# Optimization experiments

Hardware: AMD Instinct MI355X
Metric: run time of the kernel (lower is better)

The kernel has to match this reference:

```python
import jax, jax.numpy as jnp
import numpy as np

S = 4096       # sequence length
D = 1024       # d_model
H = 16         # heads
DK = 64        # d_k == d_v
VERY_SMOL_NUM = -1e9


def setup_inputs() -> dict:
    key = jax.random.key(0)
    ks = jax.random.split(key, 14)
    sd = 1.0 / np.sqrt(D)
    inp = {
        "V": jax.random.normal(ks[0], (S, D), jnp.float32),
        "K": jax.random.normal(ks[1], (S, D), jnp.float32),
        "Q": jax.random.normal(ks[2], (S, D), jnp.float32),
        # per-head projection weights, stored [in, out] (x @ W + b)
        "WQ": jax.random.normal(ks[3], (H, D, DK), jnp.float32) * sd,
        "bQ": jax.random.normal(ks[4], (H, DK), jnp.float32) * sd,
        "WK": jax.random.normal(ks[5], (H, D, DK), jnp.float32) * sd,
        "bK": jax.random.normal(ks[6], (H, DK), jnp.float32) * sd,
        "WV": jax.random.normal(ks[7], (H, D, DK), jnp.float32) * sd,
        "bV": jax.random.normal(ks[8], (H, DK), jnp.float32) * sd,
        "WO": jax.random.normal(ks[9], (D, D), jnp.float32) * sd,
        "bO": jax.random.normal(ks[10], (D,), jnp.float32) * sd,
    }
    return inp


def reference(V, K, Q, WQ, bQ, WK, bK, WV, bV, WO, bO):
    # per-head projections, vectorized over heads: [H, S, DK]
    q = jnp.einsum('sd,hdk->hsk', Q, WQ) + bQ[:, None, :]
    k = jnp.einsum('sd,hdk->hsk', K, WK) + bK[:, None, :]
    v = jnp.einsum('sd,hdk->hsk', V, WV) + bV[:, None, :]
    # full QK^T per head, scaled
    scores = jnp.einsum('hsk,htk->hst', q, k) / jnp.sqrt(jnp.float32(DK))
    # original bug faithfully preserved: with masked=True the causal additive
    # mask (triu(ones,1) * VERY_SMOL_NUM) is applied TWICE
    tri = jnp.triu(jnp.ones((S, S), jnp.float32), 1) * VERY_SMOL_NUM
    scores = scores + 2.0 * tri
    # torch Softmax(dim=1) on 2D [S,S] scores == softmax over keys (last dim)
    attn = jax.nn.softmax(scores, axis=-1)
    heads = jnp.einsum('hst,htv->hsv', attn, v)          # [H, S, DK]
    cat = heads.transpose(1, 0, 2).reshape(S, H * DK)    # concat over heads
    return cat @ WO + bO
```

## Files before the change

### kernel.cpp

```cpp
#include <hip/hip_runtime.h>

typedef unsigned short u16;
typedef unsigned int u32;
typedef __attribute__((ext_vector_type(8))) __bf16 bf16x8;
typedef __attribute__((ext_vector_type(4))) float f32x4;
typedef __attribute__((ext_vector_type(16))) float f32x16;

#define S_LEN 4096
#define D_MODEL 1024
#define NH 16
#define DHEAD 64

__device__ __forceinline__ u16 f2bf(float f){
  unsigned u = __float_as_uint(f);
  u += 0x7FFFu + ((u >> 16) & 1u);
  return (u16)(u >> 16);
}

__device__ __forceinline__ void gload_lds16(const void* g, void* l){
  __builtin_amdgcn_global_load_lds((const __attribute__((address_space(1))) void*)g,
                                   (__attribute__((address_space(3))) void*)l, 16, 0, 0);
}

__global__ __launch_bounds__(256) void cvt3_kernel(const float* __restrict__ q,
                                                   const float* __restrict__ k,
                                                   const float* __restrict__ v,
                                                   u16* __restrict__ oq,
                                                   u16* __restrict__ ok,
                                                   u16* __restrict__ ov){
  int z = blockIdx.y;
  const float* in = (z==0)? q : (z==1)? k : v;
  u16* out = (z==0)? oq : (z==1)? ok : ov;
  int i = blockIdx.x*256 + threadIdx.x;
  float4 w = reinterpret_cast<const float4*>(in)[i];
  ushort4 o;
  o.x = f2bf(w.x); o.y = f2bf(w.y); o.z = f2bf(w.z); o.w = f2bf(w.w);
  reinterpret_cast<ushort4*>(out)[i] = o;
}

__global__ __launch_bounds__(256) void tcvt_qkv_kernel(const float* __restrict__ wq,
                                                       const float* __restrict__ wk,
                                                       const float* __restrict__ wv,
                                                       u16* __restrict__ oq,
                                                       u16* __restrict__ ok,
                                                       u16* __restrict__ ov){
  int which = blockIdx.y;
  const float* in = (which==0)? wq : (which==1)? wk : wv;
  u16* out = (which==0)? oq : (which==1)? ok : ov;
  __shared__ float tile[64][67];
  int z = blockIdx.z;
  const float* inh = in + (size_t)z*1024*64;
  u16* outh = out + (size_t)z*1024*64;
  int tid = threadIdx.x;
  int r0 = blockIdx.x*64;
  #pragma unroll
  for (int c=0;c<4;c++){
    int cl = c*256 + tid;
    int row = cl >> 4, cc = (cl & 15) * 4;
    float4 v = *reinterpret_cast<const float4*>(inh + (size_t)(r0+row)*64 + cc);
    tile[row][cc+0]=v.x; tile[row][cc+1]=v.y; tile[row][cc+2]=v.z; tile[row][cc+3]=v.w;
  }
  __syncthreads();
  #pragma unroll
  for (int c=0;c<4;c++){
    int cl = c*256 + tid;
    int crow = cl >> 4, rc = (cl & 15) * 4;
    ushort4 o;
    o.x = f2bf(tile[rc+0][crow]);
    o.y = f2bf(tile[rc+1][crow]);
    o.z = f2bf(tile[rc+2][crow]);
    o.w = f2bf(tile[rc+3][crow]);
    *reinterpret_cast<ushort4*>(outh + (size_t)crow*1024 + r0 + rc) = o;
  }
}

__global__ __launch_bounds__(256) void tcvt_wo_kernel(const float* __restrict__ in,
                                                      u16* __restrict__ out){
  __shared__ float tile[64][67];
  int r0 = blockIdx.x*64, c0 = blockIdx.y*64;
  int tid = threadIdx.x;
  #pragma unroll
  for (int c=0;c<4;c++){
    int cl = c*256 + tid;
    int row = cl >> 4, cc = (cl & 15) * 4;
    float4 v = *reinterpret_cast<const float4*>(in + (size_t)(r0+row)*1024 + c0 + cc);
    tile[row][cc+0]=v.x; tile[row][cc+1]=v.y; tile[row][cc+2]=v.z; tile[row][cc+3]=v.w;
  }
  __syncthreads();
  #pragma unroll
  for (int c=0;c<4;c++){
    int cl = c*256 + tid;
    int crow = cl >> 4, rc = (cl & 15) * 4;
    ushort4 o;
    o.x = f2bf(tile[rc+0][crow]);
    o.y = f2bf(tile[rc+1][crow]);
    o.z = f2bf(tile[rc+2][crow]);
    o.w = f2bf(tile[rc+3][crow]);
    *reinterpret_cast<ushort4*>(out + (size_t)(c0+crow)*1024 + r0 + rc) = o;
  }
}

__global__ __launch_bounds__(512) void gemm_qkv_kernel(
    const u16* __restrict__ Qb, const u16* __restrict__ Kb, const u16* __restrict__ Vb,
    const u16* __restrict__ WtQ, const u16* __restrict__ WtK, const u16* __restrict__ WtV,
    const float* __restrict__ bQ, const float* __restrict__ bK, const float* __restrict__ bV,
    u16* __restrict__ qbuf, u16* __restrict__ kbuf, u16* __restrict__ vtb, float qscale){
  const int M = S_LEN, N = D_MODEL, K = D_MODEL;
  int z = blockIdx.z;
  const u16* A  = (z==0)? Qb  : (z==1)? Kb  : Vb;
  const u16* Bt = (z==0)? WtQ : (z==1)? WtK : WtV;
  const float* bias = (z==0)? bQ : (z==1)? bK : bV;
  float oscale = (z==0)? qscale : 1.0f;

  __shared__ __align__(16) unsigned char lsA[2][16384];
  __shared__ __align__(16) unsigned char lsB[2][16384];
  int tid = threadIdx.x;
  int bm = blockIdx.y * 128, bn = blockIdx.x * 128;
  int wave = tid >> 6, lane = tid & 63;
  int wm = (wave >> 1) * 32, wn = (wave & 1) * 64;
  int lrow = lane & 15, lgrp = lane >> 4;

  f32x4 acc[2][4] = {};

  auto STAGE = [&](int buf, int k0){
    #pragma unroll
    for (int c=0;c<4;c++){
      int id = c*512 + tid;
      int r = (id & 1023) >> 3;
      int kc = id & 7;
      int cs = (kc ^ (r & 7)) << 3;
      if (id < 1024)
        gload_lds16(A + (size_t)(bm+r)*K + k0 + cs, lsA[buf] + ((id & 1023) << 4));
      else
        gload_lds16(Bt + (size_t)(bn+r)*K + k0 + cs, lsB[buf] + ((id & 1023) << 4));
    }
  };

  STAGE(0, 0);
  int cur = 0;
  for (int k0 = 0; k0 < K; k0 += 64){
    __syncthreads();
    if (k0 + 64 < K) STAGE(cur^1, k0 + 64);
    #pragma unroll
    for (int ks=0;ks<2;ks++){
      bf16x8 af[2], bfr[4];
      #pragma unroll
      for (int i=0;i<2;i++){
        int ar = wm + i*16 + lrow;
        af[i] = *reinterpret_cast<const bf16x8*>(lsA[cur] + ((ar*128 + ks*64 + lgrp*16) ^ ((ar&7)<<4)));
      }
      #pragma unroll
      for (int j=0;j<4;j++){
        int br = wn + j*16 + lrow;
        bfr[j] = *reinterpret_cast<const bf16x8*>(lsB[cur] + ((br*128 + ks*64 + lgrp*16) ^ ((br&7)<<4)));
      }
      __builtin_amdgcn_s_setprio(1);
      #pragma unroll
      for (int i=0;i<2;i++)
        #pragma unroll
        for (int j=0;j<4;j++)
          acc[i][j] = __builtin_amdgcn_mfma_f32_16x16x32_bf16(af[i], bfr[j], acc[i][j], 0,0,0);
      __builtin_amdgcn_s_setprio(0);
    }
    cur ^= 1;
  }

  #pragma unroll
  for (int j=0;j<4;j++){
    int n = bn + wn + j*16 + lrow;
    float bv = bias[n];
    int hh = n >> 6, kk = n & 63;
    #pragma unroll
    for (int i=0;i<2;i++){
      int m0 = bm + wm + i*16 + lgrp*4;
      float v[4];
      #pragma unroll
      for (int r=0;r<4;r++) v[r] = (acc[i][j][r] + bv) * oscale;
      if (z < 2){
        u16* o = (z==0)? qbuf : kbuf;
        #pragma unroll
        for (int r=0;r<4;r++) o[((size_t)hh*M + m0 + r)*64 + kk] = f2bf(v[r]);
      } else {
        ushort4 p; p.x=f2bf(v[0]); p.y=f2bf(v[1]); p.z=f2bf(v[2]); p.w=f2bf(v[3]);
        *reinterpret_cast<ushort4*>(vtb + ((size_t)hh*64 + kk)*M + m0) = p;
      }
    }
  }
}

__global__ __launch_bounds__(512) void gemm_out_kernel(const u16* __restrict__ A,
                                                       const u16* __restrict__ Bt,
                                                       const float* __restrict__ bias,
                                                       float* __restrict__ dst,
                                                       int M, int N, int K){
  __shared__ __align__(16) unsigned char lsA[2][16384];
  __shared__ __align__(16) unsigned char lsB[2][16384];
  int tid = threadIdx.x;
  int bm = blockIdx.y * 128, bn = blockIdx.x * 128;
  int wave = tid >> 6, lane = tid & 63;
  int wm = (wave >> 1) * 32, wn = (wave & 1) * 64;
  int lrow = lane & 15, lgrp = lane >> 4;

  f32x4 acc[2][4] = {};

  auto STAGE = [&](int buf, int k0){
    #pragma unroll
    for (int c=0;c<4;c++){
      int id = c*512 + tid;
      int r = (id & 1023) >> 3;
      int kc = id & 7;
      int cs = (kc ^ (r & 7)) << 3;
      if (id < 1024)
        gload_lds16(A + (size_t)(bm+r)*K + k0 + cs, lsA[buf] + ((id & 1023) << 4));
      else
        gload_lds16(Bt + (size_t)(bn+r)*K + k0 + cs, lsB[buf] + ((id & 1023) << 4));
    }
  };

  STAGE(0, 0);
  int cur = 0;
  for (int k0 = 0; k0 < K; k0 += 64){
    __syncthreads();
    if (k0 + 64 < K) STAGE(cur^1, k0 + 64);
    #pragma unroll
    for (int ks=0;ks<2;ks++){
      bf16x8 af[2], bfr[4];
      #pragma unroll
      for (int i=0;i<2;i++){
        int ar = wm + i*16 + lrow;
        af[i] = *reinterpret_cast<const bf16x8*>(lsA[cur] + ((ar*128 + ks*64 + lgrp*16) ^ ((ar&7)<<4)));
      }
      #pragma unroll
      for (int j=0;j<4;j++){
        int br = wn + j*16 + lrow;
        bfr[j] = *reinterpret_cast<const bf16x8*>(lsB[cur] + ((br*128 + ks*64 + lgrp*16) ^ ((br&7)<<4)));
      }
      __builtin_amdgcn_s_setprio(1);
      #pragma unroll
      for (int i=0;i<2;i++)
        #pragma unroll
        for (int j=0;j<4;j++)
          acc[i][j] = __builtin_amdgcn_mfma_f32_16x16x32_bf16(af[i], bfr[j], acc[i][j], 0,0,0);
      __builtin_amdgcn_s_setprio(0);
    }
    cur ^= 1;
  }

  #pragma unroll
  for (int j=0;j<4;j++){
    int n = bn + wn + j*16 + lrow;
    float bv = bias[n];
    #pragma unroll
    for (int i=0;i<2;i++){
      int m0 = bm + wm + i*16 + lgrp*4;
      #pragma unroll
      for (int r=0;r<4;r++) dst[(size_t)(m0+r)*N + n] = acc[i][j][r] + bv;
    }
  }
}

__global__ __launch_bounds__(512, 2) void flash_attn_kernel(const u16* __restrict__ qb,
                                                            const u16* __restrict__ kb,
                                                            const u16* __restrict__ vtb,
                                                            u16* __restrict__ pO,
                                                            float2* __restrict__ pml){
  int b = blockIdx.x;
  int h = b & 15;
  int u = b >> 4;
  int qt = 15 - (u >> 2);
  int quarter = u & 3;
  int seg = qt + 1;
  int j0 = quarter * seg, j1 = j0 + seg;

  int tid = threadIdx.x, wave = tid >> 6, lane = tid & 63;
  int l31 = lane & 31, hi = lane >> 5;
  const u16* qh  = qb  + (size_t)h * S_LEN * 64;
  const u16* kh  = kb  + (size_t)h * S_LEN * 64;
  const u16* vth = vtb + (size_t)h * 64 * S_LEN;

  __shared__ __align__(16) unsigned char lsK[2][8192];
  __shared__ __align__(16) unsigned char lsV[2][8192];

  int qw = qt*256 + wave*32;

  bf16x8 qf[4];
  #pragma unroll
  for (int ks=0;ks<4;ks++)
    qf[ks] = *reinterpret_cast<const bf16x8*>(qh + (size_t)(qw + l31)*64 + ks*16 + hi*8);

  f32x16 oacc0 = {}, oacc1 = {};
  float m_run = -3e38f, l_run = 0.f;

  const int kvbase = hi*1024 + l31*16;
  const int krow = tid & 63, kcol = (tid >> 6) << 3;

  auto STAGE = [&](int buf, int jj){
    int kv0 = jj*64;
    gload_lds16(kh + (size_t)(kv0 + krow)*64 + kcol, lsK[buf] + (tid << 4));
    gload_lds16(vth + (size_t)krow*S_LEN + kv0 + kcol, lsV[buf] + (tid << 4));
  };

  STAGE(0, j0);
  int cur = 0;
  for (int j = j0; j < j1; j++){
    __syncthreads();
    if (j + 1 < j1) STAGE(cur^1, j + 1);

    int kv0 = j*64;
    int rel0 = qw - kv0;
    int rel1 = rel0 - 32;
    if (rel0 >= 0){
      bool act1 = rel1 >= 0;
      const unsigned char* Kc = lsK[cur] + kvbase;
      const unsigned char* Vc = lsV[cur] + kvbase;

      f32x16 s0 = {}, s1 = {};
      __builtin_amdgcn_s_setprio(1);
      #pragma unroll
      for (int ks=0;ks<4;ks++){
        bf16x8 kf = *reinterpret_cast<const bf16x8*>(Kc + ks*2048);
        s0 = __builtin_amdgcn_mfma_f32_32x32x16_bf16(kf, qf[ks], s0, 0,0,0);
      }
      if (act1){
        #pragma unroll
        for (int ks=0;ks<4;ks++){
          bf16x8 kf = *reinterpret_cast<const bf16x8*>(Kc + ks*2048 + 512);
          s1 = __builtin_amdgcn_mfma_f32_32x32x16_bf16(kf, qf[ks], s1, 0,0,0);
        }
      }
      __builtin_amdgcn_s_setprio(0);

      if (rel0 == 0){
        #pragma unroll
        for (int reg=0;reg<16;reg++){
          int kvloc = (reg & 3) + 8*(reg >> 2) + 4*hi;
          if (kvloc > l31) s0[reg] = -3e38f;
        }
      }
      if (act1 && rel1 == 0){
        #pragma unroll
        for (int reg=0;reg<16;reg++){
          int kvloc = (reg & 3) + 8*(reg >> 2) + 4*hi;
          if (kvloc > l31) s1[reg] = -3e38f;
        }
      }

      float tm[8];
      #pragma unroll
      for (int i=0;i<8;i++) tm[i] = fmaxf(s0[i], s0[i+8]);
      if (act1){
        #pragma unroll
        for (int i=0;i<8;i++) tm[i] = fmaxf(tm[i], fmaxf(s1[i], s1[i+8]));
      }
      #pragma unroll
      for (int st=4; st>=1; st>>=1){
        #pragma unroll
        for (int i=0;i<st;i++) tm[i] = fmaxf(tm[i], tm[i+st]);
      }
      float mx = fmaxf(tm[0], __shfl_xor(tm[0], 32));

      if (!__all(mx <= m_run + 11.54f)){
        float mnew = fmaxf(m_run, mx);
        float al = __builtin_amdgcn_exp2f(m_run - mnew);
        m_run = mnew; l_run *= al;
        #pragma unroll
        for (int reg=0;reg<16;reg++){ oacc0[reg] *= al; oacc1[reg] *= al; }
      }

      #pragma unroll
      for (int reg=0;reg<16;reg++) s0[reg] = __builtin_amdgcn_exp2f(s0[reg] - m_run);
      if (act1){
        #pragma unroll
        for (int reg=0;reg<16;reg++) s1[reg] = __builtin_amdgcn_exp2f(s1[reg] - m_run);
      }
      float tp[8];
      #pragma unroll
      for (int i=0;i<8;i++) tp[i] = s0[i] + s0[i+8];
      if (act1){
        #pragma unroll
        for (int i=0;i<8;i++) tp[i] += s1[i] + s1[i+8];
      }
      #pragma unroll
      for (int st=4; st>=1; st>>=1){
        #pragma unroll
        for (int i=0;i<st;i++) tp[i] += tp[i+st];
      }
      l_run += tp[0] + __shfl_xor(tp[0], 32);

      #pragma unroll
      for (int b01=0;b01<2;b01++){
        u32 A,B,C,D;
        asm("v_cvt_pk_bf16_f32 %0, %1, %2" : "=v"(A) : "v"(s0[8*b01+0]), "v"(s0[8*b01+1]));
        asm("v_cvt_pk_bf16_f32 %0, %1, %2" : "=v"(B) : "v"(s0[8*b01+2]), "v"(s0[8*b01+3]));
        asm("v_cvt_pk_bf16_f32 %0, %1, %2" : "=v"(C) : "v"(s0[8*b01+4]), "v"(s0[8*b01+5]));
        asm("v_cvt_pk_bf16_f32 %0, %1, %2" : "=v"(D) : "v"(s0[8*b01+6]), "v"(s0[8*b01+7]));
        asm("v_permlane32_swap_b32 %0, %1" : "+v"(A), "+v"(C));
        asm("v_permlane32_swap_b32 %0, %1" : "+v"(B), "+v"(D));
        union { u32 w[4]; bf16x8 v; } U;
        U.w[0]=A; U.w[1]=B; U.w[2]=C; U.w[3]=D;
        bf16x8 vf0 = *reinterpret_cast<const bf16x8*>(Vc + b01*2048);
        bf16x8 vf1 = *reinterpret_cast<const bf16x8*>(Vc + b01*2048 + 512);
        __builtin_amdgcn_s_setprio(1);
        oacc0 = __builtin_amdgcn_mfma_f32_32x32x16_bf16(vf0, U.v, oacc0, 0,0,0);
        oacc1 = __builtin_amdgcn_mfma_f32_32x32x16_bf16(vf1, U.v, oacc1, 0,0,0);
        __builtin_amdgcn_s_setprio(0);
      }
      if (act1){
        #pragma unroll
        for (int b01=0;b01<2;b01++){
          u32 A,B,C,D;
          asm("v_cvt_pk_bf16_f32 %0, %1, %2" : "=v"(A) : "v"(s1[8*b01+0]), "v"(s1[8*b01+1]));
          asm("v_cvt_pk_bf16_f32 %0, %1, %2" : "=v"(B) : "v"(s1[8*b01+2]), "v"(s1[8*b01+3]));
          asm("v_cvt_pk_bf16_f32 %0, %1, %2" : "=v"(C) : "v"(s1[8*b01+4]), "v"(s1[8*b01+5]));
          asm("v_cvt_pk_bf16_f32 %0, %1, %2" : "=v"(D) : "v"(s1[8*b01+6]), "v"(s1[8*b01+7]));
          asm("v_permlane32_swap_b32 %0, %1" : "+v"(A), "+v"(C));
          asm("v_permlane32_swap_b32 %0, %1" : "+v"(B), "+v"(D));
          union { u32 w[4]; bf16x8 v; } U;
          U.w[0]=A; U.w[1]=B; U.w[2]=C; U.w[3]=D;
          bf16x8 vf0 = *reinterpret_cast<const bf16x8*>(Vc + (2+b01)*2048);
          bf16x8 vf1 = *reinterpret_cast<const bf16x8*>(Vc + (2+b01)*2048 + 512);
          __builtin_amdgcn_s_setprio(1);
          oacc0 = __builtin_amdgcn_mfma_f32_32x32x16_bf16(vf0, U.v, oacc0, 0,0,0);
          oacc1 = __builtin_amdgcn_mfma_f32_32x32x16_bf16(vf1, U.v, oacc1, 0,0,0);
          __builtin_amdgcn_s_setprio(0);
        }
      }
    }
    cur ^= 1;
  }

  int q = qw + l31;
  if (hi == 0){
    float2 ml; ml.x = m_run; ml.y = l_run;
    pml[((size_t)quarter*NH + h)*S_LEN + q] = ml;
  }
  #pragma unroll
  for (int df=0;df<2;df++){
    #pragma unroll
    for (int q4=0;q4<4;q4++){
      float a0 = df ? oacc1[4*q4+0] : oacc0[4*q4+0];
      float a1 = df ? oacc1[4*q4+1] : oacc0[4*q4+1];
      float a2 = df ? oacc1[4*q4+2] : oacc0[4*q4+2];
      float a3 = df ? oacc1[4*q4+3] : oacc0[4*q4+3];
      u32 w0d, w1d;
      asm("v_cvt_pk_bf16_f32 %0, %1, %2" : "=v"(w0d) : "v"(a0), "v"(a1));
      asm("v_cvt_pk_bf16_f32 %0, %1, %2" : "=v"(w1d) : "v"(a2), "v"(a3));
      int dquad = df*8 + 2*q4 + hi;
      uint2 pv; pv.x = w0d; pv.y = w1d;
      *reinterpret_cast<uint2*>(pO + (((size_t)(quarter*NH + h)*16 + dquad)*S_LEN + q)*4) = pv;
    }
  }
}

__global__ __launch_bounds__(256) void combine_kernel(const u16* __restrict__ pO,
                                                      const float2* __restrict__ pml,
                                                      u16* __restrict__ catb){
  int tid = threadIdx.x;
  int dq = tid & 15, qo = tid >> 4;
  int h = blockIdx.y;
  int q = blockIdx.x*16 + qo;
  float2 ml[4];
  #pragma unroll
  for (int i=0;i<4;i++) ml[i] = pml[((size_t)i*NH + h)*S_LEN + q];
  float m = fmaxf(fmaxf(ml[0].x, ml[1].x), fmaxf(ml[2].x, ml[3].x));
  float w[4], denom = 0.f;
  #pragma unroll
  for (int i=0;i<4;i++){ w[i] = __builtin_amdgcn_exp2f(ml[i].x - m); denom += w[i]*ml[i].y; }
  float inv = 1.0f / denom;
  float x0=0.f, x1=0.f, x2=0.f, x3=0.f;
  #pragma unroll
  for (int i=0;i<4;i++){
    ushort4 a = reinterpret_cast<const ushort4*>(pO)[((size_t)i*NH*16 + (size_t)h*16 + dq)*S_LEN + q];
    x0 += __uint_as_float((u32)a.x << 16) * w[i];
    x1 += __uint_as_float((u32)a.y << 16) * w[i];
    x2 += __uint_as_float((u32)a.z << 16) * w[i];
    x3 += __uint_as_float((u32)a.w << 16) * w[i];
  }
  ushort4 o;
  o.x = f2bf(x0*inv); o.y = f2bf(x1*inv); o.z = f2bf(x2*inv); o.w = f2bf(x3*inv);
  *reinterpret_cast<ushort4*>(catb + (size_t)q*D_MODEL + h*64 + dq*4) = o;
}

extern "C" void kernel_launch(void* const* d_in, const int* in_sizes, int n_in,
                              void* d_out, int out_size, void* d_ws, size_t ws_size,
                              hipStream_t stream){
  (void)in_sizes; (void)n_in; (void)out_size; (void)ws_size;
  const float* V  = (const float*)d_in[0];
  const float* Km = (const float*)d_in[1];
  const float* Q  = (const float*)d_in[2];
  const float* WQ = (const float*)d_in[3];
  const float* bQ = (const float*)d_in[4];
  const float* WK = (const float*)d_in[5];
  const float* bK = (const float*)d_in[6];
  const float* WV = (const float*)d_in[7];
  const float* bV = (const float*)d_in[8];
  const float* WO = (const float*)d_in[9];
  const float* bO = (const float*)d_in[10];
  float* out = (float*)d_out;

  char* ws = (char*)d_ws;
  const size_t SZ_SD = (size_t)S_LEN * D_MODEL * 2;
  const size_t SZ_W  = (size_t)D_MODEL * D_MODEL * 2;
  u16* Qb   = (u16*)(ws);
  u16* Kb   = (u16*)(ws + SZ_SD);
  u16* Vb   = (u16*)(ws + 2*SZ_SD);
  u16* WtQ  = (u16*)(ws + 3*SZ_SD);
  u16* WtK  = (u16*)(ws + 3*SZ_SD + SZ_W);
  u16* WtV  = (u16*)(ws + 3*SZ_SD + 2*SZ_W);
  u16* WtO  = (u16*)(ws + 3*SZ_SD + 3*SZ_W);
  u16* qbuf = (u16*)(ws + 3*SZ_SD + 4*SZ_W);
  u16* kbuf = (u16*)(ws + 4*SZ_SD + 4*SZ_W);
  u16* vtb  = (u16*)(ws + 5*SZ_SD + 4*SZ_W);
  u16* catb = (u16*)(ws + 6*SZ_SD + 4*SZ_W);
  u16* pO   = (u16*)(ws + 7*SZ_SD + 4*SZ_W);
  float2* pml = (float2*)(ws + 11*SZ_SD + 4*SZ_W);

  const float QSCALE = 0.18033688011112042f;

  cvt3_kernel<<<dim3(4096,3),256,0,stream>>>(Q, Km, V, Qb, Kb, Vb);
  tcvt_qkv_kernel<<<dim3(16,3,16),256,0,stream>>>(WQ, WK, WV, WtQ, WtK, WtV);
  tcvt_wo_kernel<<<dim3(16,16),256,0,stream>>>(WO, WtO);
  gemm_qkv_kernel<<<dim3(8,32,3),512,0,stream>>>(Qb, Kb, Vb, WtQ, WtK, WtV,
                                                 bQ, bK, bV, qbuf, kbuf, vtb, QSCALE);
  flash_attn_kernel<<<dim3(1024),512,0,stream>>>(qbuf, kbuf, vtb, pO, pml);
  combine_kernel<<<dim3(256,16),256,0,stream>>>(pO, pml, catb);
  gemm_out_kernel<<<dim3(8,32),512,0,stream>>>(catb, WtO, bO, out, S_LEN, D_MODEL, D_MODEL);
}
```

Baseline: 153.6 us.

## Fuse fp32-to-bf16 input conversion into QKV GEMM and merge weight transposes

Drops the separate cvt3 pass over Q/K/V. The QKV GEMM now loads fp32 A tiles into registers, converts them with packed bf16 instructions and writes them to LDS, while B still streams via direct global-to-LDS loads. The three weight transpose kernels are merged into one launch. This saves a full read and write of the bf16 activation copies and two kernel launches. In exchange the GEMM reads A in fp32, which is twice the bytes, once per N-block, and uses more registers for the staged values.

```diff
diff --git a/kernel.cpp b/kernel.cpp
--- a/kernel.cpp
+++ b/kernel.cpp
@@ -22,68 +22,31 @@
                                    (__attribute__((address_space(3))) void*)l, 16, 0, 0);
 }
 
-__global__ __launch_bounds__(256) void cvt3_kernel(const float* __restrict__ q,
-                                                   const float* __restrict__ k,
-                                                   const float* __restrict__ v,
-                                                   u16* __restrict__ oq,
-                                                   u16* __restrict__ ok,
-                                                   u16* __restrict__ ov){
-  int z = blockIdx.y;
-  const float* in = (z==0)? q : (z==1)? k : v;
-  u16* out = (z==0)? oq : (z==1)? ok : ov;
-  int i = blockIdx.x*256 + threadIdx.x;
-  float4 w = reinterpret_cast<const float4*>(in)[i];
-  ushort4 o;
-  o.x = f2bf(w.x); o.y = f2bf(w.y); o.z = f2bf(w.z); o.w = f2bf(w.w);
-  reinterpret_cast<ushort4*>(out)[i] = o;
-}
-
-__global__ __launch_bounds__(256) void tcvt_qkv_kernel(const float* __restrict__ wq,
+__global__ __launch_bounds__(256) void tcvt_all_kernel(const float* __restrict__ wq,
                                                        const float* __restrict__ wk,
                                                        const float* __restrict__ wv,
+                                                       const float* __restrict__ wo,
                                                        u16* __restrict__ oq,
                                                        u16* __restrict__ ok,
-                                                       u16* __restrict__ ov){
-  int which = blockIdx.y;
-  const float* in = (which==0)? wq : (which==1)? wk : wv;
-  u16* out = (which==0)? oq : (which==1)? ok : ov;
+                                                       u16* __restrict__ ov,
+                                                       u16* __restrict__ oo){
   __shared__ float tile[64][67];
-  int z = blockIdx.z;
-  const float* inh = in + (size_t)z*1024*64;
-  u16* outh = out + (size_t)z*1024*64;
+  int y = blockIdx.y, z = blockIdx.z, x = blockIdx.x;
+  int r0 = x*64, c0;
+  const float* in; u16* out; int inStride;
+  if (y < 3){
+    in  = ((y==0)? wq : (y==1)? wk : wv) + (size_t)z*1024*64;
+    out = ((y==0)? oq : (y==1)? ok : ov) + (size_t)z*1024*64;
+    c0 = 0; inStride = 64;
+  } else {
+    in = wo; out = oo; c0 = z*64; inStride = 1024;
+  }
   int tid = threadIdx.x;
-  int r0 = blockIdx.x*64;
   #pragma unroll
   for (int c=0;c<4;c++){
     int cl = c*256 + tid;
     int row = cl >> 4, cc = (cl & 15) * 4;
-    float4 v = *reinterpret_cast<const float4*>(inh + (size_t)(r0+row)*64 + cc);
-    tile[row][cc+0]=v.x; tile[row][cc+1]=v.y; tile[row][cc+2]=v.z; tile[row][cc+3]=v.w;
-  }
-  __syncthreads();
-  #pragma unroll
-  for (int c=0;c<4;c++){
-    int cl = c*256 + tid;
-    int crow = cl >> 4, rc = (cl & 15) * 4;
-    ushort4 o;
-    o.x = f2bf(tile[rc+0][crow]);
-    o.y = f2bf(tile[rc+1][crow]);
-    o.z = f2bf(tile[rc+2][crow]);
-    o.w = f2bf(tile[rc+3][crow]);
-    *reinterpret_cast<ushort4*>(outh + (size_t)crow*1024 + r0 + rc) = o;
-  }
-}
-
-__global__ __launch_bounds__(256) void tcvt_wo_kernel(const float* __restrict__ in,
-                                                      u16* __restrict__ out){
-  __shared__ float tile[64][67];
-  int r0 = blockIdx.x*64, c0 = blockIdx.y*64;
-  int tid = threadIdx.x;
-  #pragma unroll
-  for (int c=0;c<4;c++){
-    int cl = c*256 + tid;
-    int row = cl >> 4, cc = (cl & 15) * 4;
-    float4 v = *reinterpret_cast<const float4*>(in + (size_t)(r0+row)*1024 + c0 + cc);
+    float4 v = *reinterpret_cast<const float4*>(in + (size_t)(r0+row)*inStride + c0 + cc);
     tile[row][cc+0]=v.x; tile[row][cc+1]=v.y; tile[row][cc+2]=v.z; tile[row][cc+3]=v.w;
   }
   __syncthreads();
@@ -101,14 +64,14 @@
 }
 
 __global__ __launch_bounds__(512) void gemm_qkv_kernel(
-    const u16* __restrict__ Qb, const u16* __restrict__ Kb, const u16* __restrict__ Vb,
+    const float* __restrict__ Qf, const float* __restrict__ Kf, const float* __restrict__ Vf,
     const u16* __restrict__ WtQ, const u16* __restrict__ WtK, const u16* __restrict__ WtV,
     const float* __restrict__ bQ, const float* __restrict__ bK, const float* __restrict__ bV,
     u16* __restrict__ qbuf, u16* __restrict__ kbuf, u16* __restrict__ vtb, float qscale){
   const int M = S_LEN, N = D_MODEL, K = D_MODEL;
   int z = blockIdx.z;
-  const u16* A  = (z==0)? Qb  : (z==1)? Kb  : Vb;
-  const u16* Bt = (z==0)? WtQ : (z==1)? WtK : WtV;
+  const float* Af = (z==0)? Qf  : (z==1)? Kf  : Vf;
+  const u16* Bt   = (z==0)? WtQ : (z==1)? WtK : WtV;
   const float* bias = (z==0)? bQ : (z==1)? bK : bV;
   float oscale = (z==0)? qscale : 1.0f;
 
@@ -121,26 +84,50 @@
   int lrow = lane & 15, lgrp = lane >> 4;
 
   f32x4 acc[2][4] = {};
-
-  auto STAGE = [&](int buf, int k0){
-    #pragma unroll
-    for (int c=0;c<4;c++){
-      int id = c*512 + tid;
-      int r = (id & 1023) >> 3;
-      int kc = id & 7;
+  float4 areg[2][2];
+
+  auto STAGE_B = [&](int buf, int k0){
+    #pragma unroll
+    for (int c=0;c<2;c++){
+      int u = c*512 + tid;
+      int r = u >> 3, kc = u & 7;
       int cs = (kc ^ (r & 7)) << 3;
-      if (id < 1024)
-        gload_lds16(A + (size_t)(bm+r)*K + k0 + cs, lsA[buf] + ((id & 1023) << 4));
-      else
-        gload_lds16(Bt + (size_t)(bn+r)*K + k0 + cs, lsB[buf] + ((id & 1023) << 4));
+      gload_lds16(Bt + (size_t)(bn+r)*K + k0 + cs, lsB[buf] + (u << 4));
     }
   };
-
-  STAGE(0, 0);
+  auto LOAD_A = [&](int k0){
+    #pragma unroll
+    for (int c=0;c<2;c++){
+      int u = c*512 + tid;
+      int r = u >> 3, kc = u & 7;
+      int cs = (kc ^ (r & 7)) << 3;
+      const float* src = Af + (size_t)(bm+r)*K + k0 + cs;
+      areg[c][0] = *reinterpret_cast<const float4*>(src);
+      areg[c][1] = *reinterpret_cast<const float4*>(src + 4);
+    }
+  };
+  auto WRITE_A = [&](int buf){
+    #pragma unroll
+    for (int c=0;c<2;c++){
+      int u = c*512 + tid;
+      u32 w0,w1,w2,w3;
+      asm("v_cvt_pk_bf16_f32 %0, %1, %2" : "=v"(w0) : "v"(areg[c][0].x), "v"(areg[c][0].y));
+      asm("v_cvt_pk_bf16_f32 %0, %1, %2" : "=v"(w1) : "v"(areg[c][0].z), "v"(areg[c][0].w));
+      asm("v_cvt_pk_bf16_f32 %0, %1, %2" : "=v"(w2) : "v"(areg[c][1].x), "v"(areg[c][1].y));
+      asm("v_cvt_pk_bf16_f32 %0, %1, %2" : "=v"(w3) : "v"(areg[c][1].z), "v"(areg[c][1].w));
+      uint4 pv; pv.x=w0; pv.y=w1; pv.z=w2; pv.w=w3;
+      *reinterpret_cast<uint4*>(lsA[buf] + (u << 4)) = pv;
+    }
+  };
+
+  LOAD_A(0);
+  STAGE_B(0, 0);
+  WRITE_A(0);
   int cur = 0;
   for (int k0 = 0; k0 < K; k0 += 64){
     __syncthreads();
-    if (k0 + 64 < K) STAGE(cur^1, k0 + 64);
+    bool nxt = (k0 + 64 < K);
+    if (nxt){ LOAD_A(k0 + 64); STAGE_B(cur^1, k0 + 64); }
     #pragma unroll
     for (int ks=0;ks<2;ks++){
       bf16x8 af[2], bfr[4];
@@ -162,6 +149,7 @@
           acc[i][j] = __builtin_amdgcn_mfma_f32_16x16x32_bf16(af[i], bfr[j], acc[i][j], 0,0,0);
       __builtin_amdgcn_s_setprio(0);
     }
+    if (nxt) WRITE_A(cur^1);
     cur ^= 1;
   }
 
@@ -501,26 +489,21 @@
   char* ws = (char*)d_ws;
   const size_t SZ_SD = (size_t)S_LEN * D_MODEL * 2;
   const size_t SZ_W  = (size_t)D_MODEL * D_MODEL * 2;
-  u16* Qb   = (u16*)(ws);
-  u16* Kb   = (u16*)(ws + SZ_SD);
-  u16* Vb   = (u16*)(ws + 2*SZ_SD);
-  u16* WtQ  = (u16*)(ws + 3*SZ_SD);
-  u16* WtK  = (u16*)(ws + 3*SZ_SD + SZ_W);
-  u16* WtV  = (u16*)(ws + 3*SZ_SD + 2*SZ_W);
-  u16* WtO  = (u16*)(ws + 3*SZ_SD + 3*SZ_W);
-  u16* qbuf = (u16*)(ws + 3*SZ_SD + 4*SZ_W);
-  u16* kbuf = (u16*)(ws + 4*SZ_SD + 4*SZ_W);
-  u16* vtb  = (u16*)(ws + 5*SZ_SD + 4*SZ_W);
-  u16* catb = (u16*)(ws + 6*SZ_SD + 4*SZ_W);
-  u16* pO   = (u16*)(ws + 7*SZ_SD + 4*SZ_W);
-  float2* pml = (float2*)(ws + 11*SZ_SD + 4*SZ_W);
+  u16* WtQ  = (u16*)(ws);
+  u16* WtK  = (u16*)(ws + SZ_W);
+  u16* WtV  = (u16*)(ws + 2*SZ_W);
+  u16* WtO  = (u16*)(ws + 3*SZ_W);
+  u16* qbuf = (u16*)(ws + 4*SZ_W);
+  u16* kbuf = (u16*)(ws + 4*SZ_W + SZ_SD);
+  u16* vtb  = (u16*)(ws + 4*SZ_W + 2*SZ_SD);
+  u16* catb = (u16*)(ws + 4*SZ_W + 3*SZ_SD);
+  u16* pO   = (u16*)(ws + 4*SZ_W + 4*SZ_SD);
+  float2* pml = (float2*)(ws + 4*SZ_W + 8*SZ_SD);
 
   const float QSCALE = 0.18033688011112042f;
 
-  cvt3_kernel<<<dim3(4096,3),256,0,stream>>>(Q, Km, V, Qb, Kb, Vb);
-  tcvt_qkv_kernel<<<dim3(16,3,16),256,0,stream>>>(WQ, WK, WV, WtQ, WtK, WtV);
-  tcvt_wo_kernel<<<dim3(16,16),256,0,stream>>>(WO, WtO);
-  gemm_qkv_kernel<<<dim3(8,32,3),512,0,stream>>>(Qb, Kb, Vb, WtQ, WtK, WtV,
+  tcvt_all_kernel<<<dim3(16,4,16),256,0,stream>>>(WQ, WK, WV, WO, WtQ, WtK, WtV, WtO);
+  gemm_qkv_kernel<<<dim3(8,32,3),512,0,stream>>>(Q, Km, V, WtQ, WtK, WtV,
                                                  bQ, bK, bV, qbuf, kbuf, vtb, QSCALE);
   flash_attn_kernel<<<dim3(1024),512,0,stream>>>(qbuf, kbuf, vtb, pO, pml);
   combine_kernel<<<dim3(256,16),256,0,stream>>>(pO, pml, catb);
```

Measured after the change: 157.5 us. 1.03x slower.
